# Optimization experiments

Hardware: AMD Instinct MI355X
Metric: run time of the kernel (lower is better)

Reference implementation:

```python
import jax, jax.numpy as jnp
import numpy as np

N_NODES = 50000
N_EDGES = 150000
N_TRIS = 100000
F = 256
L = 4


def setup_inputs() -> dict:
    key = jax.random.key(0)
    ks = jax.random.split(key, 8)
    x = jax.random.normal(ks[0], (N_EDGES, F), dtype=jnp.float32)
    edge_nodes = jax.random.randint(ks[1], (N_EDGES, 2), 0, N_NODES)
    tri_edges = jax.random.randint(ks[2], (N_TRIS, 3), 0, N_EDGES)
    tri_signs = (jax.random.randint(ks[3], (N_TRIS, 3), 0, 2) * 2 - 1).astype(jnp.int32)
    std = float(np.sqrt(2.0 / (F + F)))  # xavier_uniform-equivalent std
    W0_stack = jax.random.normal(ks[4], (L, F, F), dtype=jnp.float32) * std
    W1_stack = jax.random.normal(ks[5], (L, F, F), dtype=jnp.float32) * std
    W2_stack = jax.random.normal(ks[6], (L, F, F), dtype=jnp.float32) * std
    W0_L = jax.random.normal(ks[7], (F, 1), dtype=jnp.float32) * float(np.sqrt(2.0 / (F + 1)))
    return {"x": x, "W0_stack": W0_stack, "W1_stack": W1_stack, "W2_stack": W2_stack,
            "W0_L": W0_L, "edge_nodes": edge_nodes, "tri_edges": tri_edges, "tri_signs": tri_signs}


def _b1_mm(edge_nodes, y):
    # B1 @ y : [E,F] -> [N,F];  B1[u,e] = -1, B1[v,e] = +1
    u, v = edge_nodes[:, 0], edge_nodes[:, 1]
    out = jnp.zeros((N_NODES, y.shape[1]), y.dtype)
    return out.at[u].add(-y).at[v].add(y)


def _b1t_mm(edge_nodes, z):
    # B1.T @ z : [N,F] -> [E,F]
    return z[edge_nodes[:, 1]] - z[edge_nodes[:, 0]]


def _b2t_mm(tri_edges, signs, y):
    # B2.T @ y : [E,F] -> [T,F]
    return jnp.einsum('tkf,tk->tf', y[tri_edges], signs)


def _b2_mm(tri_edges, signs, w):
    # B2 @ w : [T,F] -> [E,F]
    contrib = w[:, None, :] * signs[:, :, None]  # [T,3,F]
    out = jnp.zeros((N_EDGES, w.shape[1]), w.dtype)
    return out.at[tri_edges.reshape(-1)].add(contrib.reshape(-1, w.shape[1]))


def reference(x, W0_stack, W1_stack, W2_stack, W0_L, edge_nodes, tri_edges, tri_signs):
    signs = tri_signs.astype(x.dtype)
    for i in range(L):
        d2 = _b2_mm(tri_edges, signs, _b2t_mm(tri_edges, signs, x @ W2_stack[i]))
        d1 = x @ W1_stack[i]
        d0 = _b1t_mm(edge_nodes, _b1_mm(edge_nodes, x @ W0_stack[i]))
        x = jax.nn.relu(d2 + d1 + d0)
    return _b1_mm(edge_nodes, x @ W0_L)  # [N_NODES, 1]
```

## Files before the change

### kernel.cpp

```cpp
#include <hip/hip_runtime.h>

#define M_EDGES 150000
#define NN_NODES 50000
#define N_TRIS  100000
#define F 256
#define NLAYERS 4

#define T0 1172
#define T1 391
#define T2 782
#define NTILES (T0 + T1 + T2)
#define NT_PAD 2352

typedef __attribute__((ext_vector_type(8))) __bf16 bf16x8;
typedef __attribute__((ext_vector_type(4))) float f32x4;

__device__ inline unsigned short f2bf(float f) {
    unsigned int u = __float_as_uint(f);
    u += 0x7fff + ((u >> 16) & 1);
    return (unsigned short)(u >> 16);
}
__device__ inline float bf2f(unsigned short h) {
    return __uint_as_float(((unsigned int)h) << 16);
}

__device__ inline void async16(const void* g, void* l) {
    __builtin_amdgcn_global_load_lds(
        (const __attribute__((address_space(1))) void*)g,
        (__attribute__((address_space(3))) void*)l, 16, 0, 0);
}

__global__ __launch_bounds__(256) void gemm_mfma(
    const unsigned short* __restrict__ xb,
    const unsigned short* __restrict__ sb,
    const unsigned short* __restrict__ qb,
    const unsigned short* __restrict__ wt,
    unsigned short* __restrict__ y1,
    unsigned short* __restrict__ zb,
    unsigned short* __restrict__ wb)
{
    __shared__ unsigned short As[128 * 32];
    __shared__ unsigned short Bs[128 * 32];

    const int b    = blockIdx.x;
    const int xcd  = b & 7;
    const int c    = b >> 3;
    const int tile = (c >> 1) * 8 + xcd;
    const int bn   = c & 1;
    if (tile >= NTILES) return;

    int seg, tloc;
    if (tile < T0)            { seg = 0; tloc = tile; }
    else if (tile < T0 + T1)  { seg = 1; tloc = tile - T0; }
    else                      { seg = 2; tloc = tile - T0 - T1; }
    const unsigned short* Asrc = (seg == 0) ? xb : (seg == 1) ? sb : qb;
    const int nrows = (seg == 0) ? M_EDGES : (seg == 1) ? NN_NODES : N_TRIS;
    const unsigned short* wsel = wt + seg * 65536;
    unsigned short* dst = (seg == 0) ? y1 : (seg == 1) ? zb : wb;

    const int tid  = threadIdx.x;
    const int bm0  = tloc * 128;
    const int wid  = tid >> 6;
    const int lane = tid & 63;
    const int lm   = lane & 15;
    const int lh   = lane >> 4;
    const int wm   = wid >> 1;
    const int wn   = wid & 1;
    const int wbase = tid & ~63;

    f32x4 cacc[4][4];
#pragma unroll
    for (int i = 0; i < 4; i++)
#pragma unroll
        for (int j = 0; j < 4; j++) cacc[i][j] = (f32x4){0.f, 0.f, 0.f, 0.f};

    for (int k0 = 0; k0 < 256; k0 += 32) {
#pragma unroll
        for (int s = 0; s < 2; s++) {
            int i   = s * 256 + tid;
            int row = i >> 2;
            int g   = (i & 3) ^ ((row >> 1) & 3);
            int gr  = bm0 + row;
            if (gr > nrows - 1) gr = nrows - 1;
            async16(Asrc + (size_t)gr * 256 + k0 + g * 8,
                    As + (size_t)(s * 256 + wbase) * 8);
            int nrow = bn * 128 + row;
            async16(wsel + (size_t)nrow * 256 + k0 + g * 8,
                    Bs + (size_t)(s * 256 + wbase) * 8);
        }
        asm volatile("s_waitcnt vmcnt(0)" ::: "memory");
        __syncthreads();

        bf16x8 a[4], bfr[4];
#pragma unroll
        for (int i = 0; i < 4; i++) {
            int rr = wm * 64 + i * 16 + lm;
            a[i] = *(const bf16x8*)(As + rr * 32 + ((lh ^ ((rr >> 1) & 3)) * 8));
        }
#pragma unroll
        for (int j = 0; j < 4; j++) {
            int rr = wn * 64 + j * 16 + lm;
            bfr[j] = *(const bf16x8*)(Bs + rr * 32 + ((lh ^ ((rr >> 1) & 3)) * 8));
        }
#pragma unroll
        for (int i = 0; i < 4; i++)
#pragma unroll
            for (int j = 0; j < 4; j++)
                cacc[i][j] = __builtin_amdgcn_mfma_f32_16x16x32_bf16(bfr[j], a[i], cacc[i][j], 0, 0, 0);
        __syncthreads();
    }

#pragma unroll
    for (int i = 0; i < 4; i++) {
        int grow = bm0 + wm * 64 + i * 16 + lm;
        if (grow < nrows) {
#pragma unroll
            for (int j = 0; j < 4; j++) {
                int col = bn * 128 + wn * 64 + j * 16 + lh * 4;
                ushort4 r;
                r.x = f2bf(cacc[i][j][0]);
                r.y = f2bf(cacc[i][j][1]);
                r.z = f2bf(cacc[i][j][2]);
                r.w = f2bf(cacc[i][j][3]);
                *(ushort4*)(dst + (size_t)grow * 256 + col) = r;
            }
        }
    }
}

__global__ __launch_bounds__(256) void count_nodes(
    const int* __restrict__ en, int* __restrict__ cnt)
{
    int e = blockIdx.x * 256 + threadIdx.x;
    if (e < M_EDGES) {
        atomicAdd(&cnt[en[2 * e]], 1);
        atomicAdd(&cnt[en[2 * e + 1]], 1);
    }
}

__global__ __launch_bounds__(256) void count_tris(
    const int* __restrict__ te, int* __restrict__ cnt)
{
    int t = blockIdx.x * 256 + threadIdx.x;
    if (t < N_TRIS) {
#pragma unroll
        for (int k = 0; k < 3; k++) atomicAdd(&cnt[te[3 * t + k]], 1);
    }
}

__global__ __launch_bounds__(256) void scan_block(
    const int* __restrict__ cnt, int* __restrict__ off,
    int* __restrict__ partial, int n)
{
    __shared__ int s[256];
    int t = threadIdx.x;
    int gid = blockIdx.x * 256 + t;
    int v = (gid < n) ? cnt[gid] : 0;
    s[t] = v;
    __syncthreads();
    for (int o = 1; o < 256; o <<= 1) {
        int x = (t >= o) ? s[t - o] : 0;
        __syncthreads();
        s[t] += x;
        __syncthreads();
    }
    if (gid < n) off[gid] = s[t] - v;
    if (t == 255) partial[blockIdx.x] = s[255];
}

__global__ __launch_bounds__(1024) void scan_partial(int* __restrict__ partial, int nb)
{
    __shared__ int s[1024];
    int t = threadIdx.x;
    int v = (t < nb) ? partial[t] : 0;
    s[t] = v;
    __syncthreads();
    for (int o = 1; o < 1024; o <<= 1) {
        int x = (t >= o) ? s[t - o] : 0;
        __syncthreads();
        s[t] += x;
        __syncthreads();
    }
    if (t < nb) partial[t] = s[t] - v;
}

__global__ __launch_bounds__(256) void scan_add(
    int* __restrict__ off, int* __restrict__ cursor,
    const int* __restrict__ partial, int n, int total)
{
    int gid = blockIdx.x * 256 + threadIdx.x;
    if (gid == 0) off[n] = total;
    if (gid < n) {
        int o = off[gid] + partial[blockIdx.x];
        off[gid] = o;
        cursor[gid] = o;
    }
}

__global__ __launch_bounds__(256) void fill_nodes(
    const int* __restrict__ en, int* __restrict__ cursor, int* __restrict__ adj)
{
    int e = blockIdx.x * 256 + threadIdx.x;
    if (e < M_EDGES) {
        int u = en[2 * e], v = en[2 * e + 1];
        adj[atomicAdd(&cursor[u], 1)] = (e << 1);
        adj[atomicAdd(&cursor[v], 1)] = (e << 1) | 1;
    }
}

__global__ __launch_bounds__(256) void fill_tris(
    const int* __restrict__ te, const int* __restrict__ ts,
    int* __restrict__ cursor, int* __restrict__ adj)
{
    int t = blockIdx.x * 256 + threadIdx.x;
    if (t < N_TRIS) {
#pragma unroll
        for (int k = 0; k < 3; k++) {
            int e = te[3 * t + k];
            int neg = (ts[3 * t + k] < 0) ? 1 : 0;
            adj[atomicAdd(&cursor[e], 1)] = (t << 1) | neg;
        }
    }
}

#define ZN_BLOCKS (NN_NODES / 4)
#define WT_BLOCKS (N_TRIS / 4)

__global__ __launch_bounds__(256) void agg_fused(
    const unsigned short* __restrict__ xb,
    const int* __restrict__ noff,
    const int* __restrict__ nadj,
    unsigned short* __restrict__ sbuf,
    const int* __restrict__ te,
    const int* __restrict__ ts,
    unsigned short* __restrict__ qbuf)
{
    int lane = threadIdx.x & 63;
    int f = lane * 4;
    if (blockIdx.x < ZN_BLOCKS) {
        int n = blockIdx.x * 4 + (threadIdx.x >> 6);
        int beg = noff[n], end = noff[n + 1];
        float ax = 0.f, ay = 0.f, az = 0.f, aw = 0.f;
        int i = beg;
        for (; i + 1 < end; i += 2) {
            int ea = nadj[i], eb = nadj[i + 1];
            float sa = (ea & 1) ? 1.f : -1.f;
            float sgb = (eb & 1) ? 1.f : -1.f;
            ushort4 va = *(const ushort4*)(xb + (size_t)(ea >> 1) * 256 + f);
            ushort4 vb = *(const ushort4*)(xb + (size_t)(eb >> 1) * 256 + f);
            ax += sa * bf2f(va.x) + sgb * bf2f(vb.x);
            ay += sa * bf2f(va.y) + sgb * bf2f(vb.y);
            az += sa * bf2f(va.z) + sgb * bf2f(vb.z);
            aw += sa * bf2f(va.w) + sgb * bf2f(vb.w);
        }
        if (i < end) {
            int ea = nadj[i];
            float sa = (ea & 1) ? 1.f : -1.f;
            ushort4 va = *(const ushort4*)(xb + (size_t)(ea >> 1) * 256 + f);
            ax += sa * bf2f(va.x);
            ay += sa * bf2f(va.y);
            az += sa * bf2f(va.z);
            aw += sa * bf2f(va.w);
        }
        ushort4 r;
        r.x = f2bf(ax); r.y = f2bf(ay); r.z = f2bf(az); r.w = f2bf(aw);
        *(ushort4*)(sbuf + (size_t)n * 256 + f) = r;
    } else {
        int t = (blockIdx.x - ZN_BLOCKS) * 4 + (threadIdx.x >> 6);
        int e0 = te[3 * t + 0], e1 = te[3 * t + 1], e2 = te[3 * t + 2];
        float s0 = (float)ts[3 * t + 0];
        float s1 = (float)ts[3 * t + 1];
        float s2 = (float)ts[3 * t + 2];
        ushort4 a4 = *(const ushort4*)(xb + (size_t)e0 * 256 + f);
        ushort4 b4 = *(const ushort4*)(xb + (size_t)e1 * 256 + f);
        ushort4 d4 = *(const ushort4*)(xb + (size_t)e2 * 256 + f);
        ushort4 r;
        r.x = f2bf(s0 * bf2f(a4.x) + s1 * bf2f(b4.x) + s2 * bf2f(d4.x));
        r.y = f2bf(s0 * bf2f(a4.y) + s1 * bf2f(b4.y) + s2 * bf2f(d4.y));
        r.z = f2bf(s0 * bf2f(a4.z) + s1 * bf2f(b4.z) + s2 * bf2f(d4.z));
        r.w = f2bf(s0 * bf2f(a4.w) + s1 * bf2f(b4.w) + s2 * bf2f(d4.w));
        *(ushort4*)(qbuf + (size_t)t * 256 + f) = r;
    }
}

__global__ __launch_bounds__(256) void relu_fused(
    const unsigned short* __restrict__ y1,
    const unsigned short* __restrict__ w,
    const unsigned short* __restrict__ z,
    const int* __restrict__ en,
    const int* __restrict__ eoff,
    const int* __restrict__ eadj,
    unsigned short* __restrict__ xb)
{
    int e = blockIdx.x * 4 + (threadIdx.x >> 6);
    int lane = threadIdx.x & 63;
    int f = lane * 4;
    int u = en[2 * e], v = en[2 * e + 1];
    int beg = eoff[e], end = eoff[e + 1];
    ushort4 a4 = *(const ushort4*)(y1 + (size_t)e * 256 + f);
    ushort4 zv = *(const ushort4*)(z + (size_t)v * 256 + f);
    ushort4 zu = *(const ushort4*)(z + (size_t)u * 256 + f);
    float sx = bf2f(a4.x) + bf2f(zv.x) - bf2f(zu.x);
    float sy = bf2f(a4.y) + bf2f(zv.y) - bf2f(zu.y);
    float sz = bf2f(a4.z) + bf2f(zv.z) - bf2f(zu.z);
    float sw = bf2f(a4.w) + bf2f(zv.w) - bf2f(zu.w);
    int i = beg;
    for (; i + 1 < end; i += 2) {
        int ta = eadj[i], tb = eadj[i + 1];
        float sa = (ta & 1) ? -1.f : 1.f;
        float sgb = (tb & 1) ? -1.f : 1.f;
        ushort4 wa = *(const ushort4*)(w + (size_t)(ta >> 1) * 256 + f);
        ushort4 wbv = *(const ushort4*)(w + (size_t)(tb >> 1) * 256 + f);
        sx += sa * bf2f(wa.x) + sgb * bf2f(wbv.x);
        sy += sa * bf2f(wa.y) + sgb * bf2f(wbv.y);
        sz += sa * bf2f(wa.z) + sgb * bf2f(wbv.z);
        sw += sa * bf2f(wa.w) + sgb * bf2f(wbv.w);
    }
    if (i < end) {
        int ta = eadj[i];
        float sa = (ta & 1) ? -1.f : 1.f;
        ushort4 wa = *(const ushort4*)(w + (size_t)(ta >> 1) * 256 + f);
        sx += sa * bf2f(wa.x);
        sy += sa * bf2f(wa.y);
        sz += sa * bf2f(wa.z);
        sw += sa * bf2f(wa.w);
    }
    ushort4 r;
    r.x = f2bf(fmaxf(sx, 0.f));
    r.y = f2bf(fmaxf(sy, 0.f));
    r.z = f2bf(fmaxf(sz, 0.f));
    r.w = f2bf(fmaxf(sw, 0.f));
    *(ushort4*)(xb + (size_t)e * 256 + f) = r;
}

__global__ __launch_bounds__(256) void dotp(
    const unsigned short* __restrict__ xb,
    const float* __restrict__ wl,
    float* __restrict__ p)
{
    int e = blockIdx.x * 4 + (threadIdx.x >> 6);
    int lane = threadIdx.x & 63;
    ushort4 xv = *(const ushort4*)(xb + (size_t)e * 256 + lane * 4);
    float4 wv = *(const float4*)(wl + lane * 4);
    float s = bf2f(xv.x) * wv.x + bf2f(xv.y) * wv.y +
              bf2f(xv.z) * wv.z + bf2f(xv.w) * wv.w;
#pragma unroll
    for (int off = 32; off > 0; off >>= 1)
        s += __shfl_down(s, off, 64);
    if (lane == 0) p[e] = s;
}

__global__ __launch_bounds__(256) void out_nodes(
    const float* __restrict__ p,
    const int* __restrict__ noff,
    const int* __restrict__ nadj,
    float* __restrict__ out)
{
    int n = blockIdx.x * 256 + threadIdx.x;
    if (n >= NN_NODES) return;
    int beg = noff[n], end = noff[n + 1];
    float s = 0.f;
    for (int i = beg; i < end; i++) {
        int ent = nadj[i];
        float sg = (ent & 1) ? 1.f : -1.f;
        s += sg * p[ent >> 1];
    }
    out[n] = s;
}

__global__ __launch_bounds__(256) void cvt_x(
    const float* __restrict__ x, unsigned short* __restrict__ xb)
{
    int idx = blockIdx.x * 256 + threadIdx.x;
    float4 v = *(const float4*)(x + (size_t)idx * 4);
    ushort4 r;
    r.x = f2bf(v.x); r.y = f2bf(v.y); r.z = f2bf(v.z); r.w = f2bf(v.w);
    *(ushort4*)(xb + (size_t)idx * 4) = r;
}

__global__ __launch_bounds__(256) void cvt_w(
    const float* __restrict__ W0, const float* __restrict__ W1,
    const float* __restrict__ W2, unsigned short* __restrict__ wt)
{
    int idx = blockIdx.x * 256 + threadIdx.x;
    int l = idx / (3 * 65536);
    int rem = idx - l * (3 * 65536);
    int seg = rem >> 16;
    int n = (rem >> 8) & 255;
    int k = rem & 255;
    const float* src = (seg == 0) ? W1 : (seg == 1) ? W0 : W2;
    wt[idx] = f2bf(src[(size_t)l * 65536 + k * 256 + n]);
}

extern "C" void kernel_launch(void* const* d_in, const int* in_sizes, int n_in,
                              void* d_out, int out_size, void* d_ws, size_t ws_size,
                              hipStream_t stream)
{
    const float* x0  = (const float*)d_in[0];
    const float* W0s = (const float*)d_in[1];
    const float* W1s = (const float*)d_in[2];
    const float* W2s = (const float*)d_in[3];
    const float* WL  = (const float*)d_in[4];
    const int*   en  = (const int*)d_in[5];
    const int*   te  = (const int*)d_in[6];
    const int*   ts  = (const int*)d_in[7];
    float* out = (float*)d_out;

    const size_t MF = (size_t)M_EDGES * F;
    unsigned short* xb = (unsigned short*)d_ws;
    unsigned short* y1 = xb + MF;
    unsigned short* sbuf = y1 + MF;
    unsigned short* qbuf = sbuf + (size_t)NN_NODES * 256;
    unsigned short* wt = qbuf + (size_t)N_TRIS * 256;
    unsigned short* wb = wt + (size_t)4 * 3 * 65536;
    unsigned short* zb = wb + (size_t)N_TRIS * 256;
    float* p = (float*)(zb + (size_t)NN_NODES * 256);
    int* noff = (int*)(p + M_EDGES);
    int* ncur = noff + (NN_NODES + 1);
    int* nadj = ncur + NN_NODES;
    int* eoff = nadj + 2 * M_EDGES;
    int* ecur = eoff + (M_EDGES + 1);
    int* eadj = ecur + M_EDGES;
    int* part = eadj + 3 * N_TRIS;

    cvt_w<<<(4 * 3 * 65536) / 256, 256, 0, stream>>>(W0s, W1s, W2s, wt);
    cvt_x<<<(int)(MF / 4 / 256), 256, 0, stream>>>(x0, xb);

    const int nbN = (NN_NODES + 255) / 256;
    const int nbE = (M_EDGES + 255) / 256;
    hipMemsetAsync(ncur, 0, NN_NODES * sizeof(int), stream);
    hipMemsetAsync(ecur, 0, M_EDGES * sizeof(int), stream);
    count_nodes<<<nbE, 256, 0, stream>>>(en, ncur);
    count_tris<<<(N_TRIS + 255) / 256, 256, 0, stream>>>(te, ecur);
    scan_block<<<nbN, 256, 0, stream>>>(ncur, noff, part, NN_NODES);
    scan_partial<<<1, 1024, 0, stream>>>(part, nbN);
    scan_add<<<nbN, 256, 0, stream>>>(noff, ncur, part, NN_NODES, 2 * M_EDGES);
    fill_nodes<<<nbE, 256, 0, stream>>>(en, ncur, nadj);
    scan_block<<<nbE, 256, 0, stream>>>(ecur, eoff, part, M_EDGES);
    scan_partial<<<1, 1024, 0, stream>>>(part, nbE);
    scan_add<<<nbE, 256, 0, stream>>>(eoff, ecur, part, M_EDGES, 3 * N_TRIS);
    fill_tris<<<(N_TRIS + 255) / 256, 256, 0, stream>>>(te, ts, ecur, eadj);

    const int gemm_blocks = NT_PAD * 2;
    for (int l = 0; l < NLAYERS; l++) {
        agg_fused<<<ZN_BLOCKS + WT_BLOCKS, 256, 0, stream>>>(
            xb, noff, nadj, sbuf, te, ts, qbuf);
        gemm_mfma<<<gemm_blocks, 256, 0, stream>>>(
            xb, sbuf, qbuf, wt + (size_t)l * 3 * 65536, y1, zb, wb);
        relu_fused<<<M_EDGES / 4, 256, 0, stream>>>(y1, wb, zb, en, eoff, eadj, xb);
    }

    dotp<<<M_EDGES / 4, 256, 0, stream>>>(xb, WL, p);
    out_nodes<<<(NN_NODES + 255) / 256, 256, 0, stream>>>(p, noff, nadj, out);
}
```

Measured before the change: 1.249 ms.

## Double-buffer LDS tiles in bf16 MFMA GEMM to overlap loads with compute

Splits the GEMM's shared-memory A/B tiles into two buffers. The next K-slice is issued via async global-to-LDS loads while MFMAs run on the current slice, with one wait and barrier per step instead of load-wait-compute serialization. It also raises wave priority around the MFMA block with s_setprio. The cost is doubled LDS use per block, which may reduce occupancy, and more complex barrier ordering.

```diff
diff --git a/kernel.cpp b/kernel.cpp
--- a/kernel.cpp
+++ b/kernel.cpp
@@ -39,8 +39,10 @@
     unsigned short* __restrict__ zb,
     unsigned short* __restrict__ wb)
 {
-    __shared__ unsigned short As[128 * 32];
-    __shared__ unsigned short Bs[128 * 32];
+    __shared__ unsigned short As0[128 * 32];
+    __shared__ unsigned short As1[128 * 32];
+    __shared__ unsigned short Bs0[128 * 32];
+    __shared__ unsigned short Bs1[128 * 32];
 
     const int b    = blockIdx.x;
     const int xcd  = b & 7;
@@ -74,41 +76,71 @@
 #pragma unroll
         for (int j = 0; j < 4; j++) cacc[i][j] = (f32x4){0.f, 0.f, 0.f, 0.f};
 
-    for (int k0 = 0; k0 < 256; k0 += 32) {
-#pragma unroll
-        for (int s = 0; s < 2; s++) {
-            int i   = s * 256 + tid;
-            int row = i >> 2;
-            int g   = (i & 3) ^ ((row >> 1) & 3);
-            int gr  = bm0 + row;
-            if (gr > nrows - 1) gr = nrows - 1;
-            async16(Asrc + (size_t)gr * 256 + k0 + g * 8,
-                    As + (size_t)(s * 256 + wbase) * 8);
-            int nrow = bn * 128 + row;
-            async16(wsel + (size_t)nrow * 256 + k0 + g * 8,
-                    Bs + (size_t)(s * 256 + wbase) * 8);
-        }
-        asm volatile("s_waitcnt vmcnt(0)" ::: "memory");
-        __syncthreads();
-
-        bf16x8 a[4], bfr[4];
-#pragma unroll
-        for (int i = 0; i < 4; i++) {
-            int rr = wm * 64 + i * 16 + lm;
-            a[i] = *(const bf16x8*)(As + rr * 32 + ((lh ^ ((rr >> 1) & 3)) * 8));
-        }
-#pragma unroll
-        for (int j = 0; j < 4; j++) {
-            int rr = wn * 64 + j * 16 + lm;
-            bfr[j] = *(const bf16x8*)(Bs + rr * 32 + ((lh ^ ((rr >> 1) & 3)) * 8));
-        }
-#pragma unroll
-        for (int i = 0; i < 4; i++)
-#pragma unroll
-            for (int j = 0; j < 4; j++)
-                cacc[i][j] = __builtin_amdgcn_mfma_f32_16x16x32_bf16(bfr[j], a[i], cacc[i][j], 0, 0, 0);
-        __syncthreads();
-    }
+#define STAGE(Ad, Bd, k0)                                                   \
+    do {                                                                    \
+        _Pragma("unroll")                                                   \
+        for (int ss = 0; ss < 2; ss++) {                                    \
+            int ii  = ss * 256 + tid;                                       \
+            int row = ii >> 2;                                              \
+            int g   = (ii & 3) ^ ((row >> 1) & 3);                          \
+            int gr  = bm0 + row;                                            \
+            if (gr > nrows - 1) gr = nrows - 1;                             \
+            async16(Asrc + (size_t)gr * 256 + (k0) + g * 8,                 \
+                    Ad + (size_t)(ss * 256 + wbase) * 8);                   \
+            int nrow = bn * 128 + row;                                      \
+            async16(wsel + (size_t)nrow * 256 + (k0) + g * 8,               \
+                    Bd + (size_t)(ss * 256 + wbase) * 8);                   \
+        }                                                                   \
+    } while (0)
+
+#define COMPUTE(Ad, Bd)                                                     \
+    do {                                                                    \
+        bf16x8 a[4], bfr[4];                                                \
+        _Pragma("unroll")                                                   \
+        for (int i = 0; i < 4; i++) {                                       \
+            int rr = wm * 64 + i * 16 + lm;                                 \
+            a[i] = *(const bf16x8*)(Ad + rr * 32 +                          \
+                                    ((lh ^ ((rr >> 1) & 3)) * 8));          \
+        }                                                                   \
+        _Pragma("unroll")                                                   \
+        for (int j = 0; j < 4; j++) {                                       \
+            int rr = wn * 64 + j * 16 + lm;                                 \
+            bfr[j] = *(const bf16x8*)(Bd + rr * 32 +                        \
+                                      ((lh ^ ((rr >> 1) & 3)) * 8));        \
+        }                                                                   \
+        __builtin_amdgcn_s_setprio(1);                                      \
+        _Pragma("unroll")                                                   \
+        for (int i = 0; i < 4; i++)                                         \
+            _Pragma("unroll")                                               \
+            for (int j = 0; j < 4; j++)                                     \
+                cacc[i][j] = __builtin_amdgcn_mfma_f32_16x16x32_bf16(       \
+                    bfr[j], a[i], cacc[i][j], 0, 0, 0);                     \
+        __builtin_amdgcn_s_setprio(0);                                      \
+    } while (0)
+
+#define WAITBAR()                                                           \
+    do {                                                                    \
+        asm volatile("s_waitcnt vmcnt(0)" ::: "memory");                    \
+        __builtin_amdgcn_s_barrier();                                       \
+        asm volatile("" ::: "memory");                                      \
+    } while (0)
+
+    STAGE(As0, Bs0, 0);
+    WAITBAR();
+
+#pragma unroll
+    for (int kk = 0; kk < 8; kk += 2) {
+        if (kk + 1 < 8) STAGE(As1, Bs1, (kk + 1) * 32);
+        COMPUTE(As0, Bs0);
+        WAITBAR();
+        if (kk + 2 < 8) STAGE(As0, Bs0, (kk + 2) * 32);
+        COMPUTE(As1, Bs1);
+        if (kk + 2 < 8) WAITBAR();
+    }
+
+#undef STAGE
+#undef COMPUTE
+#undef WAITBAR
 
 #pragma unroll
     for (int i = 0; i < 4; i++) {
```

New measurement: 1.246 ms. About the same (-0.2%).

## Widen GEMM tiles to full 256 columns, remap tiles per XCD, fuse dot-product into last ReLU

Applied to the files above, without the earlier changes.

The MFMA GEMM now uses 512-thread blocks that compute a full 128x256 output tile, so each A tile is loaded once instead of twice. Tile indices are laid out as contiguous ranges per XCD. The final-layer relu_fused kernel computes the W0_L dot product directly, which removes the separate dotp kernel and the last write and reread of xb. The larger block doubles B-tile LDS use and lowers per-block parallelism.

```diff
diff --git a/kernel.cpp b/kernel.cpp
--- a/kernel.cpp
+++ b/kernel.cpp
@@ -11,6 +11,7 @@
 #define T2 782
 #define NTILES (T0 + T1 + T2)
 #define NT_PAD 2352
+#define TPX 294
 
 typedef __attribute__((ext_vector_type(8))) __bf16 bf16x8;
 typedef __attribute__((ext_vector_type(4))) float f32x4;
@@ -30,7 +31,7 @@
         (__attribute__((address_space(3))) void*)l, 16, 0, 0);
 }
 
-__global__ __launch_bounds__(256) void gemm_mfma(
+__global__ __launch_bounds__(512) void gemm_mfma(
     const unsigned short* __restrict__ xb,
     const unsigned short* __restrict__ sb,
     const unsigned short* __restrict__ qb,
@@ -40,13 +41,12 @@
     unsigned short* __restrict__ wb)
 {
     __shared__ unsigned short As[128 * 32];
-    __shared__ unsigned short Bs[128 * 32];
+    __shared__ unsigned short Bs[256 * 32];
 
     const int b    = blockIdx.x;
     const int xcd  = b & 7;
-    const int c    = b >> 3;
-    const int tile = (c >> 1) * 8 + xcd;
-    const int bn   = c & 1;
+    const int idx  = b >> 3;
+    const int tile = xcd * TPX + idx;
     if (tile >= NTILES) return;
 
     int seg, tloc;
@@ -64,8 +64,8 @@
     const int lane = tid & 63;
     const int lm   = lane & 15;
     const int lh   = lane >> 4;
-    const int wm   = wid >> 1;
-    const int wn   = wid & 1;
+    const int wm   = wid >> 2;
+    const int wn   = wid & 3;
     const int wbase = tid & ~63;
 
     f32x4 cacc[4][4];
@@ -75,18 +75,21 @@
         for (int j = 0; j < 4; j++) cacc[i][j] = (f32x4){0.f, 0.f, 0.f, 0.f};
 
     for (int k0 = 0; k0 < 256; k0 += 32) {
-#pragma unroll
-        for (int s = 0; s < 2; s++) {
-            int i   = s * 256 + tid;
-            int row = i >> 2;
-            int g   = (i & 3) ^ ((row >> 1) & 3);
+        {
+            int row = tid >> 2;
+            int g   = (tid & 3) ^ ((row >> 1) & 3);
             int gr  = bm0 + row;
             if (gr > nrows - 1) gr = nrows - 1;
             async16(Asrc + (size_t)gr * 256 + k0 + g * 8,
-                    As + (size_t)(s * 256 + wbase) * 8);
-            int nrow = bn * 128 + row;
-            async16(wsel + (size_t)nrow * 256 + k0 + g * 8,
-                    Bs + (size_t)(s * 256 + wbase) * 8);
+                    As + (size_t)wbase * 8);
+        }
+#pragma unroll
+        for (int ss = 0; ss < 2; ss++) {
+            int i   = ss * 512 + tid;
+            int row = i >> 2;
+            int g   = (i & 3) ^ ((row >> 1) & 3);
+            async16(wsel + (size_t)row * 256 + k0 + g * 8,
+                    Bs + (size_t)(ss * 512 + wbase) * 8);
         }
         asm volatile("s_waitcnt vmcnt(0)" ::: "memory");
         __syncthreads();
@@ -106,7 +109,8 @@
         for (int i = 0; i < 4; i++)
 #pragma unroll
             for (int j = 0; j < 4; j++)
-                cacc[i][j] = __builtin_amdgcn_mfma_f32_16x16x32_bf16(bfr[j], a[i], cacc[i][j], 0, 0, 0);
+                cacc[i][j] = __builtin_amdgcn_mfma_f32_16x16x32_bf16(
+                    bfr[j], a[i], cacc[i][j], 0, 0, 0);
         __syncthreads();
     }
 
@@ -116,7 +120,7 @@
         if (grow < nrows) {
 #pragma unroll
             for (int j = 0; j < 4; j++) {
-                int col = bn * 128 + wn * 64 + j * 16 + lh * 4;
+                int col = wn * 64 + j * 16 + lh * 4;
                 ushort4 r;
                 r.x = f2bf(cacc[i][j][0]);
                 r.y = f2bf(cacc[i][j][1]);
@@ -290,7 +294,10 @@
     const int* __restrict__ en,
     const int* __restrict__ eoff,
     const int* __restrict__ eadj,
-    unsigned short* __restrict__ xb)
+    unsigned short* __restrict__ xb,
+    const float* __restrict__ wl,
+    float* __restrict__ p,
+    int last)
 {
     int e = blockIdx.x * 4 + (threadIdx.x >> 6);
     int lane = threadIdx.x & 63;
@@ -325,29 +332,22 @@
         sz += sa * bf2f(wa.z);
         sw += sa * bf2f(wa.w);
     }
-    ushort4 r;
-    r.x = f2bf(fmaxf(sx, 0.f));
-    r.y = f2bf(fmaxf(sy, 0.f));
-    r.z = f2bf(fmaxf(sz, 0.f));
-    r.w = f2bf(fmaxf(sw, 0.f));
-    *(ushort4*)(xb + (size_t)e * 256 + f) = r;
-}
-
-__global__ __launch_bounds__(256) void dotp(
-    const unsigned short* __restrict__ xb,
-    const float* __restrict__ wl,
-    float* __restrict__ p)
-{
-    int e = blockIdx.x * 4 + (threadIdx.x >> 6);
-    int lane = threadIdx.x & 63;
-    ushort4 xv = *(const ushort4*)(xb + (size_t)e * 256 + lane * 4);
-    float4 wv = *(const float4*)(wl + lane * 4);
-    float s = bf2f(xv.x) * wv.x + bf2f(xv.y) * wv.y +
-              bf2f(xv.z) * wv.z + bf2f(xv.w) * wv.w;
-#pragma unroll
-    for (int off = 32; off > 0; off >>= 1)
-        s += __shfl_down(s, off, 64);
-    if (lane == 0) p[e] = s;
+    sx = fmaxf(sx, 0.f);
+    sy = fmaxf(sy, 0.f);
+    sz = fmaxf(sz, 0.f);
+    sw = fmaxf(sw, 0.f);
+    if (!last) {
+        ushort4 r;
+        r.x = f2bf(sx); r.y = f2bf(sy); r.z = f2bf(sz); r.w = f2bf(sw);
+        *(ushort4*)(xb + (size_t)e * 256 + f) = r;
+    } else {
+        float4 wv = *(const float4*)(wl + f);
+        float s = sx * wv.x + sy * wv.y + sz * wv.z + sw * wv.w;
+#pragma unroll
+        for (int off = 32; off > 0; off >>= 1)
+            s += __shfl_down(s, off, 64);
+        if (lane == 0) p[e] = s;
+    }
 }
 
 __global__ __launch_bounds__(256) void out_nodes(
@@ -441,15 +441,14 @@
     scan_add<<<nbE, 256, 0, stream>>>(eoff, ecur, part, M_EDGES, 3 * N_TRIS);
     fill_tris<<<(N_TRIS + 255) / 256, 256, 0, stream>>>(te, ts, ecur, eadj);
 
-    const int gemm_blocks = NT_PAD * 2;
     for (int l = 0; l < NLAYERS; l++) {
         agg_fused<<<ZN_BLOCKS + WT_BLOCKS, 256, 0, stream>>>(
             xb, noff, nadj, sbuf, te, ts, qbuf);
-        gemm_mfma<<<gemm_blocks, 256, 0, stream>>>(
+        gemm_mfma<<<NT_PAD, 512, 0, stream>>>(
             xb, sbuf, qbuf, wt + (size_t)l * 3 * 65536, y1, zb, wb);
-        relu_fused<<<M_EDGES / 4, 256, 0, stream>>>(y1, wb, zb, en, eoff, eadj, xb);
-    }
-
-    dotp<<<M_EDGES / 4, 256, 0, stream>>>(xb, WL, p);
+        relu_fused<<<M_EDGES / 4, 256, 0, stream>>>(
+            y1, wb, zb, en, eoff, eadj, xb, WL, p, (l == NLAYERS - 1) ? 1 : 0);
+    }
+
     out_nodes<<<(NN_NODES + 255) / 256, 256, 0, stream>>>(p, noff, nadj, out);
 }
```

After: 1.241 ms. No clear change (-0.6%).
